# Kernel optimization log

Hardware: AMD Instinct MI355X
Metric: run time of the kernel (lower is better)

## Reference

```python
import jax, jax.numpy as jnp
import numpy as np

N_HEAD = 16
HEAD_DIM = 64
N_EMBD = N_HEAD * HEAD_DIM
KS, STRIDE = 4, 4
LN_EPS = 1e-5


def _layernorm(x, g, b):
    mu = jnp.mean(x, axis=-1, keepdims=True)
    var = jnp.var(x, axis=-1, keepdims=True)
    return (x - mu) * jax.lax.rsqrt(var + LN_EPS) * g + b


def _depthwise_conv(x_bcl, w):
    # x_bcl: [N, head_dim, L], w: [head_dim, 1, KS] (torch Conv1d groups=head_dim layout)
    return jax.lax.conv_general_dilated(
        x_bcl, w, window_strides=(STRIDE,), padding='VALID',
        dimension_numbers=('NCH', 'OIH', 'NCH'), feature_group_count=HEAD_DIM)


def setup_inputs() -> dict:
    key = jax.random.key(0)
    ks = jax.random.split(key, 12)
    B, T, L = 8, 64, 4096
    s = 0.02
    return {
        'x': jax.random.normal(ks[0], (B, T, N_EMBD), jnp.float32),
        'cached_k': jax.random.normal(ks[1], (B, N_HEAD, L, HEAD_DIM), jnp.float32),
        'cached_v': jax.random.normal(ks[2], (B, N_HEAD, L, HEAD_DIM), jnp.float32),
        'w_attn': jax.random.normal(ks[3], (N_EMBD, 3 * N_EMBD), jnp.float32) * s,
        'b_attn': jnp.zeros((3 * N_EMBD,), jnp.float32),
        'w_proj': jax.random.normal(ks[4], (N_EMBD, N_EMBD), jnp.float32) * s,
        'b_proj': jnp.zeros((N_EMBD,), jnp.float32),
        'k_conv': jax.random.normal(ks[5], (HEAD_DIM, 1, KS), jnp.float32) * 0.5,
        'v_conv': jax.random.normal(ks[6], (HEAD_DIM, 1, KS), jnp.float32) * 0.5,
        'ln_k_g': jnp.ones((HEAD_DIM,), jnp.float32),
        'ln_k_b': jnp.zeros((HEAD_DIM,), jnp.float32),
        'ln_v_g': jnp.ones((HEAD_DIM,), jnp.float32),
        'ln_v_b': jnp.zeros((HEAD_DIM,), jnp.float32),
    }


def reference(x, cached_k, cached_v, w_attn, b_attn, w_proj, b_proj,
              k_conv, v_conv, ln_k_g, ln_k_b, ln_v_g, ln_v_b):
    B, T, C = x.shape
    H, hd = N_HEAD, HEAD_DIM
    qkv = x @ w_attn + b_attn                      # [B,T,3C]
    q, k, v = jnp.split(qkv, 3, axis=-1)
    q = q.reshape(B, T, H, hd).transpose(0, 2, 1, 3)  # [B,H,T,hd]
    k = k.reshape(B, T, H, hd).transpose(0, 2, 1, 3)
    v = v.reshape(B, T, H, hd).transpose(0, 2, 1, 3)

    # compress cached K/V: depthwise conv over cache length, then LayerNorm
    L = cached_k.shape[2]
    pk = cached_k.transpose(0, 1, 3, 2).reshape(B * H, hd, L)
    pv = cached_v.transpose(0, 1, 3, 2).reshape(B * H, hd, L)
    ck = _depthwise_conv(pk, k_conv).reshape(B, H, hd, -1).transpose(0, 1, 3, 2)  # [B,H,Lc,hd]
    cv = _depthwise_conv(pv, v_conv).reshape(B, H, hd, -1).transpose(0, 1, 3, 2)
    ck = jax.lax.stop_gradient(_layernorm(ck, ln_k_g, ln_k_b))
    cv = jax.lax.stop_gradient(_layernorm(cv, ln_v_g, ln_v_b))

    k_full = jnp.concatenate([ck, k], axis=2)      # [B,H,Tk,hd]
    v_full = jnp.concatenate([cv, v], axis=2)
    Tk = k_full.shape[2]

    # faithful to original: rectangular tril(T, Tk) -> query i sees keys j<=i
    mask = jnp.tril(jnp.ones((T, Tk), dtype=bool))
    att = jnp.einsum('bhqd,bhkd->bhqk', q, k_full) * (1.0 / np.sqrt(hd))
    att = jnp.where(mask[None, None], att, -jnp.inf)
    att = jax.nn.softmax(att, axis=-1)
    y = jnp.einsum('bhqk,bhkd->bhqd', att, v_full)
    y = y.transpose(0, 2, 1, 3).reshape(B, T, C)
    return y @ w_proj + b_proj
```

## Files before the change

kernel.cpp:

```cpp
#include <hip/hip_runtime.h>
#include <math.h>

#define NH 16
#define LCACHE 4096

typedef __attribute__((ext_vector_type(8))) short short8;
typedef __attribute__((ext_vector_type(8))) unsigned short ushort8;
typedef __attribute__((ext_vector_type(4))) float f32x4;

__device__ __forceinline__ unsigned short f2bf(float f) {
    unsigned int u = __float_as_uint(f);
    u = (u + 0x7fffu + ((u >> 16) & 1u)) >> 16;
    return (unsigned short)u;
}
__device__ __forceinline__ void gload16(const ushort* g, ushort* l) {
    __builtin_amdgcn_global_load_lds((const __attribute__((address_space(1))) void*)g,
                                     (__attribute__((address_space(3))) void*)l, 16, 0, 0);
}
__device__ __forceinline__ void stage6(const ushort* agb, const ushort* bgb,
                                       ushort* stgb, int buf, int kt, int w4, int l)
{
    const ushort* ga = agb + (size_t)kt * 2048 + w4 * 512 + l * 8;
    const ushort* gb = bgb + (size_t)kt * 4096 + w4 * 1024 + l * 8;
    ushort* la = stgb + buf * 6144 + w4 * 512;
    ushort* lb = stgb + buf * 6144 + 2048 + w4 * 1024;
    gload16(ga, la); gload16(gb, lb); gload16(gb + 512, lb + 512);
}

__global__ __launch_bounds__(256)
void prep_kernel(const float* __restrict__ cached_k, const float* __restrict__ cached_v,
                 const float* __restrict__ kcw, const float* __restrict__ vcw,
                 const float* __restrict__ lkg, const float* __restrict__ lkb,
                 const float* __restrict__ lvg, const float* __restrict__ lvb,
                 const float* __restrict__ x, const float* __restrict__ w_attn,
                 const float* __restrict__ w_proj,
                 ushort* __restrict__ ckf, ushort* __restrict__ cvtf,
                 ushort* __restrict__ xp, ushort* __restrict__ wq,
                 ushort* __restrict__ wp)
{
    __shared__ float Wt[64][65];
    const int bid = blockIdx.x, tid = threadIdx.x;
    const int w = tid >> 6, l = tid & 63;

    const int isP = (bid >= 256);
    const int g2  = bid & 255;
    const int ntw = g2 >> 4, ktw = g2 & 15;
    const float* W = isP ? w_proj : w_attn;
    const int ldw  = isP ? 1024 : 3072;
    ushort* D      = isP ? wp : wq;
    float wreg[16];
#pragma unroll
    for (int rep = 0; rep < 16; ++rep) {
        int lin = rep * 256 + tid;
        int kr = lin >> 6, nn = lin & 63;
        wreg[rep] = W[(size_t)(ktw * 64 + kr) * ldw + ntw * 64 + nn];
    }

    {
        const int bh = bid >> 2, sub = bid & 3;
        const int T = sub >> 1, half = sub & 1;
        const float* S = (T ? cached_v : cached_k) + (size_t)bh * (LCACHE * 64);
        const float* cwp = T ? vcw : kcw;
        float4 w4v = *(const float4*)(cwp + l * 4);
        float g = (T ? lvg : lkg)[l], bb = (T ? lvb : lkb)[l];
        ushort* dstf = (T ? cvtf : ckf) + (size_t)bh * 4096;
#pragma unroll
        for (int it = 0; it < 2; ++it) {
            float av[4];
#pragma unroll
            for (int q = 0; q < 4; ++q) {
                int key = half * 32 + w * 8 + it * 4 + q;
                const float* p = S + (size_t)key * 256 + l;
                float acc = p[0] * w4v.x;
                acc = fmaf(p[64],  w4v.y, acc);
                acc = fmaf(p[128], w4v.z, acc);
                acc = fmaf(p[192], w4v.w, acc);
                av[q] = acc;
            }
            float s1[4], s2[4];
#pragma unroll
            for (int q = 0; q < 4; ++q) { s1[q] = av[q]; s2[q] = av[q] * av[q]; }
#pragma unroll
            for (int o = 32; o; o >>= 1) {
#pragma unroll
                for (int q = 0; q < 4; ++q) {
                    s1[q] += __shfl_xor(s1[q], o);
                    s2[q] += __shfl_xor(s2[q], o);
                }
            }
#pragma unroll
            for (int q = 0; q < 4; ++q) {
                int key = half * 32 + w * 8 + it * 4 + q;
                float mu  = s1[q] * 0.015625f;
                float var = s2[q] * 0.015625f - mu * mu;
                float outv = (av[q] - mu) * rsqrtf(var + 1e-5f) * g + bb;
                const int d = l;
                int off;
                if (T)
                    off = ((d >> 4) * 2 + (key >> 5)) * 512
                        + ((key >> 3) & 3) * 128 + (d & 15) * 8 + (key & 7);
                else
                    off = ((key >> 4) * 2 + (d >> 5)) * 512
                        + ((d >> 3) & 3) * 128 + (key & 15) * 8 + (d & 7);
                dstf[off] = f2bf(outv);
            }
        }
    }

    {
#pragma unroll
        for (int rep = 0; rep < 16; ++rep) {
            int lin = rep * 256 + tid;
            Wt[lin >> 6][lin & 63] = wreg[rep];
        }
        __syncthreads();
        int r = l & 15, kg8 = l >> 4;
#pragma unroll
        for (int e = 0; e < 2; ++e) {
            int bi = w + e * 4;
            int kb = bi >> 2, nb = bi & 3;
            ushort8 o;
#pragma unroll
            for (int j = 0; j < 8; ++j)
                o[j] = f2bf(Wt[kb * 32 + kg8 * 8 + j][nb * 16 + r]);
            size_t f_lin = (size_t)(ntw * 16 + ktw) * 8 + bi;
            *(ushort8*)(D + f_lin * 512 + l * 8) = o;
        }
    }

    if (bid < 64) {
        int r = l & 15, kg8 = l >> 4;
#pragma unroll
        for (int i = 0; i < 4; ++i) {
            int f = bid * 16 + w * 4 + i;
            int mt = f >> 6, kt = (f >> 2) & 15, fi = f & 3;
            int kb = fi >> 1, mb = fi & 1;
            int m  = mt * 32 + mb * 16 + r;
            int k0 = kt * 64 + kb * 32 + kg8 * 8;
            const float* s = x + (size_t)m * 1024 + k0;
            ushort8 o;
#pragma unroll
            for (int j = 0; j < 8; ++j) o[j] = f2bf(s[j]);
            *(ushort8*)(xp + (size_t)f * 512 + l * 8) = o;
        }
    }
}

__global__ __launch_bounds__(512)
void attn_kernel(const ushort* __restrict__ ckf, const ushort* __restrict__ cvtf,
                 const float* __restrict__ b_attn,
                 const ushort* __restrict__ xp, const ushort* __restrict__ wq,
                 ushort* __restrict__ yp)
{
    __shared__ __align__(16) ushort stg[2][4][6144];
    __shared__ __align__(16) float qs[32][68];
    __shared__ __align__(16) ushort P_lds[32 * 64];

    const int bid = blockIdx.x;
    const int h    = ((bid & 7) << 1) | ((bid >> 3) & 1);
    const int rem  = bid >> 4;
    const int b    = rem >> 1;
    const int half = rem & 1;
    const int mtA  = b * 2 + half;

    const int tid = threadIdx.x;
    const int w = tid >> 6, l = tid & 63;
    const int kg = w >> 2, w4 = w & 3;
    const int c = l & 15, rg = l >> 4;

    const ushort* agb = xp + (size_t)mtA * 32768;
    const ushort* bgb = wq + (size_t)h * 65536;
    ushort* stgb = &stg[kg][0][0];
    stage6(agb, bgb, stgb, 0, kg * 8 + 0, w4, l);
    stage6(agb, bgb, stgb, 1, kg * 8 + 1, w4, l);
    stage6(agb, bgb, stgb, 2, kg * 8 + 2, w4, l);

    f32x4 acc0 = {0.f,0.f,0.f,0.f}, acc1 = {0.f,0.f,0.f,0.f};
#pragma unroll
    for (int s = 0; s < 8; ++s) {
        if (s < 6)       asm volatile("s_waitcnt vmcnt(6)" ::: "memory");
        else if (s == 6) asm volatile("s_waitcnt vmcnt(3)" ::: "memory");
        else             asm volatile("s_waitcnt vmcnt(0)" ::: "memory");
        __builtin_amdgcn_s_barrier();
        if (s < 5) stage6(agb, bgb, stgb, (s + 3) & 3, kg * 8 + s + 3, w4, l);
        const ushort* La = stgb + (s & 3) * 6144;
        const ushort* Lb = La + 2048;
        short8 b0  = *(const short8*)(Lb + (size_t)w4 * 512 + l * 8);
        short8 a00 = *(const short8*)(La + (size_t)l * 8);
        short8 a01 = *(const short8*)(La + 512 + (size_t)l * 8);
        acc0 = __builtin_amdgcn_mfma_f32_16x16x32_bf16(a00, b0, acc0, 0, 0, 0);
        acc1 = __builtin_amdgcn_mfma_f32_16x16x32_bf16(a01, b0, acc1, 0, 0, 0);
        short8 b1  = *(const short8*)(Lb + (size_t)(4 + w4) * 512 + l * 8);
        short8 a10 = *(const short8*)(La + 1024 + (size_t)l * 8);
        short8 a11 = *(const short8*)(La + 1536 + (size_t)l * 8);
        acc0 = __builtin_amdgcn_mfma_f32_16x16x32_bf16(a10, b1, acc0, 0, 0, 0);
        acc1 = __builtin_amdgcn_mfma_f32_16x16x32_bf16(a11, b1, acc1, 0, 0, 0);
    }

    {
        const int n = w4 * 16 + c;
        if (kg == 0) {
#pragma unroll
            for (int mb = 0; mb < 2; ++mb) {
                f32x4 acc = mb ? acc1 : acc0;
#pragma unroll
                for (int rr = 0; rr < 4; ++rr)
                    qs[mb * 16 + rg * 4 + rr][n] = acc[rr];
            }
        }
        __syncthreads();
        if (kg == 1) {
            float bv = b_attn[h * 64 + n];
#pragma unroll
            for (int mb = 0; mb < 2; ++mb) {
                f32x4 acc = mb ? acc1 : acc0;
#pragma unroll
                for (int rr = 0; rr < 4; ++rr) {
                    int m = mb * 16 + rg * 4 + rr;
                    qs[m][n] = (qs[m][n] + acc[rr] + bv) * 0.125f;
                }
            }
        }
        __syncthreads();
    }

    const int g = w & 1, dup = w >> 1;
    const ushort* ckb = ckf + (size_t)(b * NH + h) * 4096;
    const ushort* cvb = cvtf + (size_t)(b * NH + h) * 4096;

    short8 akf[4][2];
#pragma unroll
    for (int mf = 0; mf < 4; ++mf)
#pragma unroll
        for (int kf = 0; kf < 2; ++kf)
            akf[mf][kf] = *(const short8*)(ckb + (mf * 2 + kf) * 512 + l * 8);

    short8 qb[2];
#pragma unroll
    for (int kf = 0; kf < 2; ++kf) {
        int row = 16 * g + c;
        int d0  = 32 * kf + 8 * rg;
        float4 v0 = *(const float4*)&qs[row][d0];
        float4 v1 = *(const float4*)&qs[row][d0 + 4];
        ushort8 t;
        t[0] = f2bf(v0.x); t[1] = f2bf(v0.y); t[2] = f2bf(v0.z); t[3] = f2bf(v0.w);
        t[4] = f2bf(v1.x); t[5] = f2bf(v1.y); t[6] = f2bf(v1.z); t[7] = f2bf(v1.w);
        qb[kf] = (short8)t;
    }

    f32x4 sacc[4];
#pragma unroll
    for (int mf = 0; mf < 4; ++mf) { sacc[mf][0]=0.f; sacc[mf][1]=0.f; sacc[mf][2]=0.f; sacc[mf][3]=0.f; }
#pragma unroll
    for (int mf = 0; mf < 4; ++mf) {
        sacc[mf] = __builtin_amdgcn_mfma_f32_16x16x32_bf16(akf[mf][0], qb[0], sacc[mf], 0, 0, 0);
        sacc[mf] = __builtin_amdgcn_mfma_f32_16x16x32_bf16(akf[mf][1], qb[1], sacc[mf], 0, 0, 0);
    }

    const int gq = half * 32 + 16 * g + c;
    float pv[4][4];
    float mx = -3.0e38f;
#pragma unroll
    for (int mf = 0; mf < 4; ++mf)
#pragma unroll
        for (int rr = 0; rr < 4; ++rr) {
            int kidx = 16 * mf + 4 * rg + rr;
            float sc = (kidx <= gq) ? sacc[mf][rr] : -3.0e38f;
            pv[mf][rr] = sc;
            mx = fmaxf(mx, sc);
        }
    mx = fmaxf(mx, __shfl_xor(mx, 16));
    mx = fmaxf(mx, __shfl_xor(mx, 32));
    float sum = 0.f;
#pragma unroll
    for (int mf = 0; mf < 4; ++mf)
#pragma unroll
        for (int rr = 0; rr < 4; ++rr) {
            int kidx = 16 * mf + 4 * rg + rr;
            float e = (kidx <= gq) ? __expf(pv[mf][rr] - mx) : 0.f;
            pv[mf][rr] = e;
            sum += e;
        }
    sum += __shfl_xor(sum, 16);
    sum += __shfl_xor(sum, 32);
    float inv = 1.0f / sum;

    if (dup == 0) {
        int q = 16 * g + c;
        int swz = (q & 7) << 3;
#pragma unroll
        for (int mf = 0; mf < 4; ++mf)
#pragma unroll
            for (int rr = 0; rr < 4; ++rr) {
                int kidx = 16 * mf + 4 * rg + rr;
                P_lds[q * 64 + (kidx ^ swz)] = f2bf(pv[mf][rr] * inv);
            }
    }
    __syncthreads();

    short8 avf[2], pb[2];
#pragma unroll
    for (int kf = 0; kf < 2; ++kf) {
        avf[kf] = *(const short8*)(cvb + (dup * 2 + kf) * 512 + l * 8);
        int q = 16 * g + c;
        int key0 = 32 * kf + 8 * rg;
        pb[kf] = *(const short8*)&P_lds[q * 64 + (key0 ^ ((q & 7) << 3))];
    }
    f32x4 oacc = {0.f, 0.f, 0.f, 0.f};
    oacc = __builtin_amdgcn_mfma_f32_16x16x32_bf16(avf[0], pb[0], oacc, 0, 0, 0);
    oacc = __builtin_amdgcn_mfma_f32_16x16x32_bf16(avf[1], pb[1], oacc, 0, 0, 0);

#pragma unroll
    for (int rr = 0; rr < 4; ++rr) {
        int d  = 16 * dup + 4 * rg + rr;
        int kb = d >> 5, ke = d & 31;
        int l2 = ((ke >> 3) << 4) | c;
        int j2 = ke & 7;
        size_t off = (size_t)mtA * 32768 + (size_t)h * 2048
                   + (size_t)(kb * 2 + g) * 512 + (size_t)l2 * 8 + j2;
        yp[off] = f2bf(oacc[rr]);
    }
}

__global__ __launch_bounds__(512)
void gemm2_kernel(const ushort* __restrict__ Ap, const ushort* __restrict__ Bp,
                  const float* __restrict__ bias, float* __restrict__ C)
{
    __shared__ __align__(16) ushort stg[2][4][6144];
    __shared__ float red[32][68];

    const int bid = blockIdx.x;
    const int nt = ((bid & 7) << 1) | ((bid >> 3) & 1);
    const int mt = bid >> 4;
    const int tid = threadIdx.x;
    const int w = tid >> 6, l = tid & 63;
    const int kg = w >> 2, w4 = w & 3;

    const ushort* agb = Ap + (size_t)mt * 32768;
    const ushort* bgb = Bp + (size_t)nt * 65536;
    ushort* stgb = &stg[kg][0][0];
    stage6(agb, bgb, stgb, 0, kg * 8 + 0, w4, l);
    stage6(agb, bgb, stgb, 1, kg * 8 + 1, w4, l);
    stage6(agb, bgb, stgb, 2, kg * 8 + 2, w4, l);

    f32x4 acc0 = {0.f,0.f,0.f,0.f}, acc1 = {0.f,0.f,0.f,0.f};
#pragma unroll
    for (int s = 0; s < 8; ++s) {
        if (s < 6)       asm volatile("s_waitcnt vmcnt(6)" ::: "memory");
        else if (s == 6) asm volatile("s_waitcnt vmcnt(3)" ::: "memory");
        else             asm volatile("s_waitcnt vmcnt(0)" ::: "memory");
        __builtin_amdgcn_s_barrier();
        if (s < 5) stage6(agb, bgb, stgb, (s + 3) & 3, kg * 8 + s + 3, w4, l);
        const ushort* La = stgb + (s & 3) * 6144;
        const ushort* Lb = La + 2048;
        short8 b0  = *(const short8*)(Lb + (size_t)w4 * 512 + l * 8);
        short8 a00 = *(const short8*)(La + (size_t)l * 8);
        short8 a01 = *(const short8*)(La + 512 + (size_t)l * 8);
        acc0 = __builtin_amdgcn_mfma_f32_16x16x32_bf16(a00, b0, acc0, 0, 0, 0);
        acc1 = __builtin_amdgcn_mfma_f32_16x16x32_bf16(a01, b0, acc1, 0, 0, 0);
        short8 b1  = *(const short8*)(Lb + (size_t)(4 + w4) * 512 + l * 8);
        short8 a10 = *(const short8*)(La + 1024 + (size_t)l * 8);
        short8 a11 = *(const short8*)(La + 1536 + (size_t)l * 8);
        acc0 = __builtin_amdgcn_mfma_f32_16x16x32_bf16(a10, b1, acc0, 0, 0, 0);
        acc1 = __builtin_amdgcn_mfma_f32_16x16x32_bf16(a11, b1, acc1, 0, 0, 0);
    }

    const int c = l & 15, rg = l >> 4;
    const int nl = w4 * 16 + c;
    if (kg == 0) {
#pragma unroll
        for (int mb = 0; mb < 2; ++mb) {
            f32x4 acc = mb ? acc1 : acc0;
#pragma unroll
            for (int rr = 0; rr < 4; ++rr)
                red[mb * 16 + rg * 4 + rr][nl] = acc[rr];
        }
    }
    __syncthreads();
    if (kg == 1) {
        float bv = bias[nt * 64 + nl];
#pragma unroll
        for (int mb = 0; mb < 2; ++mb) {
            f32x4 acc = mb ? acc1 : acc0;
#pragma unroll
            for (int rr = 0; rr < 4; ++rr) {
                int m = mb * 16 + rg * 4 + rr;
                C[(size_t)(mt * 32 + m) * 1024 + nt * 64 + nl] =
                    red[m][nl] + acc[rr] + bv;
            }
        }
    }
}

extern "C" void kernel_launch(void* const* d_in, const int* in_sizes, int n_in,
                              void* d_out, int out_size, void* d_ws, size_t ws_size,
                              hipStream_t stream)
{
    const float* x        = (const float*)d_in[0];
    const float* cached_k = (const float*)d_in[1];
    const float* cached_v = (const float*)d_in[2];
    const float* w_attn   = (const float*)d_in[3];
    const float* b_attn   = (const float*)d_in[4];
    const float* w_proj   = (const float*)d_in[5];
    const float* b_proj   = (const float*)d_in[6];
    const float* k_conv   = (const float*)d_in[7];
    const float* v_conv   = (const float*)d_in[8];
    const float* ln_k_g   = (const float*)d_in[9];
    const float* ln_k_b   = (const float*)d_in[10];
    const float* ln_v_g   = (const float*)d_in[11];
    const float* ln_v_b   = (const float*)d_in[12];

    ushort* xp   = (ushort*)d_ws;
    ushort* wq   = xp + 524288;
    ushort* wp   = wq + 1048576;
    ushort* yp   = wp + 1048576;
    ushort* ckf  = yp + 524288;
    ushort* cvtf = ckf + 524288;
    float* out   = (float*)d_out;

    prep_kernel<<<512, 256, 0, stream>>>(cached_k, cached_v, k_conv, v_conv,
                                         ln_k_g, ln_k_b, ln_v_g, ln_v_b,
                                         x, w_attn, w_proj, ckf, cvtf, xp, wq, wp);
    attn_kernel<<<256, 512, 0, stream>>>(ckf, cvtf, b_attn, xp, wq, yp);
    gemm2_kernel<<<256, 512, 0, stream>>>(yp, wp, b_proj, out);
}
```

Measured before the change: 28.23 us.

## Replace LDS-staged GEMM pipelines with direct global register loads and hoist early loads

Both GEMM loops (QKV projection in attn_kernel and output projection in gemm2_kernel) drop the global_load_lds multi-buffered LDS staging with waitcnt and barriers, and instead load packed bf16 fragments straight from global memory into registers. This removes barrier sync and the large LDS footprint, which together with launch_bounds(512,2) aims for higher occupancy. Compressed K/V fragment loads in attn_kernel and the conv tap loads in prep_kernel are moved to the start so their latency overlaps the other work. The cost is more register pressure and no explicit prefetch pipeline, so global load latency becomes exposed in the GEMM loop.

```diff
diff --git a/kernel.cpp b/kernel.cpp
--- a/kernel.cpp
+++ b/kernel.cpp
@@ -12,19 +12,6 @@
     unsigned int u = __float_as_uint(f);
     u = (u + 0x7fffu + ((u >> 16) & 1u)) >> 16;
     return (unsigned short)u;
-}
-__device__ __forceinline__ void gload16(const ushort* g, ushort* l) {
-    __builtin_amdgcn_global_load_lds((const __attribute__((address_space(1))) void*)g,
-                                     (__attribute__((address_space(3))) void*)l, 16, 0, 0);
-}
-__device__ __forceinline__ void stage6(const ushort* agb, const ushort* bgb,
-                                       ushort* stgb, int buf, int kt, int w4, int l)
-{
-    const ushort* ga = agb + (size_t)kt * 2048 + w4 * 512 + l * 8;
-    const ushort* gb = bgb + (size_t)kt * 4096 + w4 * 1024 + l * 8;
-    ushort* la = stgb + buf * 6144 + w4 * 512;
-    ushort* lb = stgb + buf * 6144 + 2048 + w4 * 1024;
-    gload16(ga, la); gload16(gb, lb); gload16(gb + 512, lb + 512);
 }
 
 __global__ __launch_bounds__(256)
@@ -42,6 +29,17 @@
     const int bid = blockIdx.x, tid = threadIdx.x;
     const int w = tid >> 6, l = tid & 63;
 
+    const int bh = bid >> 2, sub = bid & 3;
+    const int T = sub >> 1, half = sub & 1;
+    const float* S = (T ? cached_v : cached_k) + (size_t)bh * (LCACHE * 64);
+    float tap[8][4];
+#pragma unroll
+    for (int rq = 0; rq < 8; ++rq) {
+        int key = half * 32 + w * 8 + rq;
+        const float* p = S + (size_t)key * 256 + l;
+        tap[rq][0] = p[0]; tap[rq][1] = p[64]; tap[rq][2] = p[128]; tap[rq][3] = p[192];
+    }
+
     const int isP = (bid >= 256);
     const int g2  = bid & 255;
     const int ntw = g2 >> 4, ktw = g2 & 15;
@@ -57,9 +55,6 @@
     }
 
     {
-        const int bh = bid >> 2, sub = bid & 3;
-        const int T = sub >> 1, half = sub & 1;
-        const float* S = (T ? cached_v : cached_k) + (size_t)bh * (LCACHE * 64);
         const float* cwp = T ? vcw : kcw;
         float4 w4v = *(const float4*)(cwp + l * 4);
         float g = (T ? lvg : lkg)[l], bb = (T ? lvb : lkb)[l];
@@ -69,12 +64,11 @@
             float av[4];
 #pragma unroll
             for (int q = 0; q < 4; ++q) {
-                int key = half * 32 + w * 8 + it * 4 + q;
-                const float* p = S + (size_t)key * 256 + l;
-                float acc = p[0] * w4v.x;
-                acc = fmaf(p[64],  w4v.y, acc);
-                acc = fmaf(p[128], w4v.z, acc);
-                acc = fmaf(p[192], w4v.w, acc);
+                int rq = it * 4 + q;
+                float acc = tap[rq][0] * w4v.x;
+                acc = fmaf(tap[rq][1], w4v.y, acc);
+                acc = fmaf(tap[rq][2], w4v.z, acc);
+                acc = fmaf(tap[rq][3], w4v.w, acc);
                 av[q] = acc;
             }
             float s1[4], s2[4];
@@ -146,13 +140,12 @@
     }
 }
 
-__global__ __launch_bounds__(512)
+__global__ __launch_bounds__(512, 2)
 void attn_kernel(const ushort* __restrict__ ckf, const ushort* __restrict__ cvtf,
                  const float* __restrict__ b_attn,
                  const ushort* __restrict__ xp, const ushort* __restrict__ wq,
                  ushort* __restrict__ yp)
 {
-    __shared__ __align__(16) ushort stg[2][4][6144];
     __shared__ __align__(16) float qs[32][68];
     __shared__ __align__(16) ushort P_lds[32 * 64];
 
@@ -167,32 +160,37 @@
     const int w = tid >> 6, l = tid & 63;
     const int kg = w >> 2, w4 = w & 3;
     const int c = l & 15, rg = l >> 4;
-
-    const ushort* agb = xp + (size_t)mtA * 32768;
-    const ushort* bgb = wq + (size_t)h * 65536;
-    ushort* stgb = &stg[kg][0][0];
-    stage6(agb, bgb, stgb, 0, kg * 8 + 0, w4, l);
-    stage6(agb, bgb, stgb, 1, kg * 8 + 1, w4, l);
-    stage6(agb, bgb, stgb, 2, kg * 8 + 2, w4, l);
-
+    const int g = w & 1, dup = w >> 1;
+
+    const ushort* ckb = ckf + (size_t)(b * NH + h) * 4096;
+    const ushort* cvb = cvtf + (size_t)(b * NH + h) * 4096;
+    short8 akf[4][2];
+#pragma unroll
+    for (int mf = 0; mf < 4; ++mf)
+#pragma unroll
+        for (int kf = 0; kf < 2; ++kf)
+            akf[mf][kf] = *(const short8*)(ckb + (mf * 2 + kf) * 512 + l * 8);
+    short8 avf[2];
+#pragma unroll
+    for (int kf = 0; kf < 2; ++kf)
+        avf[kf] = *(const short8*)(cvb + (dup * 2 + kf) * 512 + l * 8);
+
+    const ushort* ab = xp + (size_t)mtA * 32768;
+    const ushort* bb = wq + (size_t)h * 65536;
     f32x4 acc0 = {0.f,0.f,0.f,0.f}, acc1 = {0.f,0.f,0.f,0.f};
 #pragma unroll
     for (int s = 0; s < 8; ++s) {
-        if (s < 6)       asm volatile("s_waitcnt vmcnt(6)" ::: "memory");
-        else if (s == 6) asm volatile("s_waitcnt vmcnt(3)" ::: "memory");
-        else             asm volatile("s_waitcnt vmcnt(0)" ::: "memory");
-        __builtin_amdgcn_s_barrier();
-        if (s < 5) stage6(agb, bgb, stgb, (s + 3) & 3, kg * 8 + s + 3, w4, l);
-        const ushort* La = stgb + (s & 3) * 6144;
-        const ushort* Lb = La + 2048;
-        short8 b0  = *(const short8*)(Lb + (size_t)w4 * 512 + l * 8);
-        short8 a00 = *(const short8*)(La + (size_t)l * 8);
-        short8 a01 = *(const short8*)(La + 512 + (size_t)l * 8);
+        const int kt = kg * 8 + s;
+        const ushort* A = ab + kt * 2048;
+        const ushort* B = bb + kt * 4096;
+        short8 a00 = *(const short8*)(A + l * 8);
+        short8 a01 = *(const short8*)(A + 512 + l * 8);
+        short8 a10 = *(const short8*)(A + 1024 + l * 8);
+        short8 a11 = *(const short8*)(A + 1536 + l * 8);
+        short8 b0  = *(const short8*)(B + (size_t)w4 * 512 + l * 8);
+        short8 b1  = *(const short8*)(B + (size_t)(4 + w4) * 512 + l * 8);
         acc0 = __builtin_amdgcn_mfma_f32_16x16x32_bf16(a00, b0, acc0, 0, 0, 0);
         acc1 = __builtin_amdgcn_mfma_f32_16x16x32_bf16(a01, b0, acc1, 0, 0, 0);
-        short8 b1  = *(const short8*)(Lb + (size_t)(4 + w4) * 512 + l * 8);
-        short8 a10 = *(const short8*)(La + 1024 + (size_t)l * 8);
-        short8 a11 = *(const short8*)(La + 1536 + (size_t)l * 8);
         acc0 = __builtin_amdgcn_mfma_f32_16x16x32_bf16(a10, b1, acc0, 0, 0, 0);
         acc1 = __builtin_amdgcn_mfma_f32_16x16x32_bf16(a11, b1, acc1, 0, 0, 0);
     }
@@ -223,17 +221,6 @@
         }
         __syncthreads();
     }
-
-    const int g = w & 1, dup = w >> 1;
-    const ushort* ckb = ckf + (size_t)(b * NH + h) * 4096;
-    const ushort* cvb = cvtf + (size_t)(b * NH + h) * 4096;
-
-    short8 akf[4][2];
-#pragma unroll
-    for (int mf = 0; mf < 4; ++mf)
-#pragma unroll
-        for (int kf = 0; kf < 2; ++kf)
-            akf[mf][kf] = *(const short8*)(ckb + (mf * 2 + kf) * 512 + l * 8);
 
     short8 qb[2];
 #pragma unroll
@@ -298,10 +285,9 @@
     }
     __syncthreads();
 
-    short8 avf[2], pb[2];
+    short8 pb[2];
 #pragma unroll
     for (int kf = 0; kf < 2; ++kf) {
-        avf[kf] = *(const short8*)(cvb + (dup * 2 + kf) * 512 + l * 8);
         int q = 16 * g + c;
         int key0 = 32 * kf + 8 * rg;
         pb[kf] = *(const short8*)&P_lds[q * 64 + (key0 ^ ((q & 7) << 3))];
@@ -322,11 +308,10 @@
     }
 }
 
-__global__ __launch_bounds__(512)
+__global__ __launch_bounds__(512, 2)
 void gemm2_kernel(const ushort* __restrict__ Ap, const ushort* __restrict__ Bp,
                   const float* __restrict__ bias, float* __restrict__ C)
 {
-    __shared__ __align__(16) ushort stg[2][4][6144];
     __shared__ float red[32][68];
 
     const int bid = blockIdx.x;
@@ -335,37 +320,28 @@
     const int tid = threadIdx.x;
     const int w = tid >> 6, l = tid & 63;
     const int kg = w >> 2, w4 = w & 3;
-
-    const ushort* agb = Ap + (size_t)mt * 32768;
-    const ushort* bgb = Bp + (size_t)nt * 65536;
-    ushort* stgb = &stg[kg][0][0];
-    stage6(agb, bgb, stgb, 0, kg * 8 + 0, w4, l);
-    stage6(agb, bgb, stgb, 1, kg * 8 + 1, w4, l);
-    stage6(agb, bgb, stgb, 2, kg * 8 + 2, w4, l);
-
+    const int c = l & 15, rg = l >> 4;
+
+    const ushort* ab = Ap + (size_t)mt * 32768;
+    const ushort* bb = Bp + (size_t)nt * 65536;
     f32x4 acc0 = {0.f,0.f,0.f,0.f}, acc1 = {0.f,0.f,0.f,0.f};
 #pragma unroll
     for (int s = 0; s < 8; ++s) {
-        if (s < 6)       asm volatile("s_waitcnt vmcnt(6)" ::: "memory");
-        else if (s == 6) asm volatile("s_waitcnt vmcnt(3)" ::: "memory");
-        else             asm volatile("s_waitcnt vmcnt(0)" ::: "memory");
-        __builtin_amdgcn_s_barrier();
-        if (s < 5) stage6(agb, bgb, stgb, (s + 3) & 3, kg * 8 + s + 3, w4, l);
-        const ushort* La = stgb + (s & 3) * 6144;
-        const ushort* Lb = La + 2048;
-        short8 b0  = *(const short8*)(Lb + (size_t)w4 * 512 + l * 8);
-        short8 a00 = *(const short8*)(La + (size_t)l * 8);
-        short8 a01 = *(const short8*)(La + 512 + (size_t)l * 8);
+        const int kt = kg * 8 + s;
+        const ushort* A = ab + kt * 2048;
+        const ushort* B = bb + kt * 4096;
+        short8 a00 = *(const short8*)(A + l * 8);
+        short8 a01 = *(const short8*)(A + 512 + l * 8);
+        short8 a10 = *(const short8*)(A + 1024 + l * 8);
+        short8 a11 = *(const short8*)(A + 1536 + l * 8);
+        short8 b0  = *(const short8*)(B + (size_t)w4 * 512 + l * 8);
+        short8 b1  = *(const short8*)(B + (size_t)(4 + w4) * 512 + l * 8);
         acc0 = __builtin_amdgcn_mfma_f32_16x16x32_bf16(a00, b0, acc0, 0, 0, 0);
         acc1 = __builtin_amdgcn_mfma_f32_16x16x32_bf16(a01, b0, acc1, 0, 0, 0);
-        short8 b1  = *(const short8*)(Lb + (size_t)(4 + w4) * 512 + l * 8);
-        short8 a10 = *(const short8*)(La + 1024 + (size_t)l * 8);
-        short8 a11 = *(const short8*)(La + 1536 + (size_t)l * 8);
         acc0 = __builtin_amdgcn_mfma_f32_16x16x32_bf16(a10, b1, acc0, 0, 0, 0);
         acc1 = __builtin_amdgcn_mfma_f32_16x16x32_bf16(a11, b1, acc1, 0, 0, 0);
     }
 
-    const int c = l & 15, rg = l >> 4;
     const int nl = w4 * 16 + c;
     if (kg == 0) {
 #pragma unroll
```

Measured after the change: 26.88 us. 4.8% less time.
